# Kernel optimization log

Hardware: AMD Instinct MI355X
Metric: run time of the kernel (lower is better)

## Reference

```python
import jax, jax.numpy as jnp
import numpy as np

W = 256  # sliding_window_size


def setup_inputs() -> dict:
    key = jax.random.key(0)
    x = jax.random.normal(key, (2, 16, 4096, 64), dtype=jnp.float32)
    return {"x": x}


def _sliding_qk(q, k, w):
    """Banded QK^T, faithful to Longformer sliding_chunks_matmul_qk.
    q, k: [P, S, D]. Returns [P, S, 2w+1] with -inf at out-of-range band positions.
    """
    P, S, D = q.shape
    n = S // w  # number of w-sized chunks
    qc = q.reshape(P, n, w, D)
    # each query chunk i attends to keys in [(i-1)*w, (i+2)*w): a 3w halo window
    kp = jnp.pad(k, ((0, 0), (w, w), (0, 0)))  # pad value irrelevant, masked below
    idx = jnp.arange(n)[:, None] * w + jnp.arange(3 * w)[None, :]  # [n, 3w]
    kc = kp[:, idx, :]  # [P, n, 3w, D]
    scores = jnp.einsum('pnxd,pnyd->pnxy', qc, kc)  # [P, n, w, 3w]
    # band extraction: for row x in a chunk, offset c in [0, 2w] sits at column x + c
    gidx = jnp.arange(w)[:, None] + jnp.arange(2 * w + 1)[None, :]  # [w, 2w+1]
    band = jnp.take_along_axis(scores, gidx[None, None], axis=-1)  # [P, n, w, 2w+1]
    band = band.reshape(P, S, 2 * w + 1)
    # mask positions where key index j = i + c - w falls outside [0, S)
    i = jnp.arange(S)[:, None]
    c = jnp.arange(2 * w + 1)[None, :]
    j = i + c - w
    valid = (j >= 0) & (j < S)  # [S, 2w+1]
    return jnp.where(valid[None], band, -jnp.inf)


def reference(x):
    B, H, S, D = x.shape
    w = W
    # faithful to the torch code: transpose(1,2) then flat reshape to (B*H, S, D)
    qr = jnp.transpose(x, (0, 2, 1, 3)).reshape(B * H, S, D)
    scores = _sliding_qk(qr, qr, w)  # [B*H, S, 2w+1]
    scores = scores.reshape(B, H, S, 2 * w + 1).transpose(0, 2, 1, 3)  # [B, S, H, 2w+1]
    probs = jax.nn.softmax(scores.astype(jnp.float32), axis=-1)
    return probs.astype(x.dtype)  # dropout p=0.0 -> identity
```

## Files before the change

kernel.cpp:

```cpp
#include <hip/hip_runtime.h>
#include <math.h>

#define S_LEN 4096
#define NHEAD 16
#define WI    256
#define NC    513
#define TI    64
#define CK    96
#define NCH   6
#define NT    36
#define KSTR  72
#define PV    (S_LEN * 64)

typedef __attribute__((ext_vector_type(8))) short short8;
typedef __attribute__((ext_vector_type(4))) float floatx4;

static __device__ __forceinline__ unsigned short f2bf_rn(float f) {
  unsigned int u = __float_as_uint(f);
  u += 0x7FFFu + ((u >> 16) & 1u);
  return (unsigned short)(u >> 16);
}

__global__ __launch_bounds__(256)
void split_kernel(const float* __restrict__ x,
                  unsigned short* __restrict__ xh,
                  unsigned short* __restrict__ xl) {
  const int idx = blockIdx.x * 256 + threadIdx.x;
  const float4 val = ((const float4*)x)[idx];
  const int d4  = idx & 15;
  const int row = idx >> 4;
  const int s = row & 4095;
  const int h = (row >> 12) & 15;
  const int b = row >> 16;
  const int p = (b << 4) + (s >> 8);
  const int v = ((s & 255) << 4) + h;
  const size_t off = (size_t)p * PV + v * 64 + d4 * 4;
  const unsigned int ux = __float_as_uint(val.x), uy = __float_as_uint(val.y);
  const unsigned int uz = __float_as_uint(val.z), uw = __float_as_uint(val.w);
  ushort4 hi, lo;
  hi.x = ux >> 16; hi.y = uy >> 16; hi.z = uz >> 16; hi.w = uw >> 16;
  lo.x = f2bf_rn(val.x - __uint_as_float(ux & 0xFFFF0000u));
  lo.y = f2bf_rn(val.y - __uint_as_float(uy & 0xFFFF0000u));
  lo.z = f2bf_rn(val.z - __uint_as_float(uz & 0xFFFF0000u));
  lo.w = f2bf_rn(val.w - __uint_as_float(uw & 0xFFFF0000u));
  *(ushort4*)(xh + off) = hi;
  *(ushort4*)(xl + off) = lo;
}

__global__ __launch_bounds__(256, 2)
void attn_kernel(const unsigned short* __restrict__ xh,
                 const unsigned short* __restrict__ xl,
                 float* __restrict__ out) {
  const int t  = threadIdx.x;
  const int id = blockIdx.x;
  const int p    = id >> 6;
  const int r6   = id & 63;
  const int tile = ((r6 & 7) << 3) | (r6 >> 3);
  const int i0   = tile * TI;
  const int b    = p >> 4;
  const int hh   = p & 15;
  const int jb   = i0 - WI;
  const int w    = t >> 6;
  const int quad = (t >> 4) & 3;
  const int n    = t & 15;

  __shared__ unsigned short Qh[TI * KSTR], Ql[TI * KSTR];
  __shared__ unsigned short Kh[CK * KSTR], Kl[CK * KSTR];

  const unsigned short* ph = xh + (size_t)p * PV;
  const unsigned short* pl = xl + (size_t)p * PV;

#define LOAD_CHUNK(mm, dsth, dstl)                                      \
  { _Pragma("unroll")                                                   \
    for (int k = 0; k < 3; ++k) {                                       \
      const int u = t + (k << 8);                                       \
      const int row = u >> 3, col = (u & 7) << 3;                       \
      const int v = jb + (mm) * CK + row;                               \
      short8 zh = {0,0,0,0,0,0,0,0}, zl = {0,0,0,0,0,0,0,0};            \
      if (v >= 0 && v < S_LEN) {                                        \
        zh = *(const short8*)(ph + (size_t)v * 64 + col);               \
        zl = *(const short8*)(pl + (size_t)v * 64 + col);               \
      }                                                                 \
      (dsth)[k] = zh; (dstl)[k] = zl;                                   \
    } }

#define WRITE_CHUNK(srch, srcl)                                         \
  { _Pragma("unroll")                                                   \
    for (int k = 0; k < 3; ++k) {                                       \
      const int u = t + (k << 8);                                       \
      const int row = u >> 3, col = (u & 7) << 3;                       \
      *(short8*)(Kh + row * KSTR + col) = (srch)[k];                    \
      *(short8*)(Kl + row * KSTR + col) = (srcl)[k];                    \
    } }

  short8 qbh[2], qbl[2];
#pragma unroll
  for (int k = 0; k < 2; ++k) {
    const int u = t + (k << 8);
    const int row = u >> 3, col = (u & 7) << 3;
    qbh[k] = *(const short8*)(ph + (size_t)(i0 + row) * 64 + col);
    qbl[k] = *(const short8*)(pl + (size_t)(i0 + row) * 64 + col);
  }
  short8 pfh[2][3], pfl[2][3];
  LOAD_CHUNK(0, pfh[0], pfl[0]);
#pragma unroll
  for (int k = 0; k < 2; ++k) {
    const int u = t + (k << 8);
    const int row = u >> 3, col = (u & 7) << 3;
    *(short8*)(Qh + row * KSTR + col) = qbh[k];
    *(short8*)(Ql + row * KSTR + col) = qbl[k];
  }
  __syncthreads();

  const int arow = (w * 16 + n) * KSTR + quad * 8;
  const short8 qh0 = *(const short8*)(Qh + arow);
  const short8 qh1 = *(const short8*)(Qh + arow + 32);
  const short8 ql0 = *(const short8*)(Ql + arow);
  const short8 ql1 = *(const short8*)(Ql + arow + 32);

  floatx4 acc[NT];
#pragma unroll
  for (int jt = 0; jt < NT; ++jt) acc[jt] = (floatx4){0.f, 0.f, 0.f, 0.f};

#pragma unroll
  for (int m = 0; m < NCH; ++m) {
    WRITE_CHUNK(pfh[m & 1], pfl[m & 1]);
    __syncthreads();
    if (m < NCH - 1) LOAD_CHUNK(m + 1, pfh[(m + 1) & 1], pfl[(m + 1) & 1]);
#pragma unroll
    for (int u = 0; u < 6; ++u) {
      const int jt = m * 6 + u;
      const int kbase = (u * 16 + n) * KSTR + quad * 8;
      const short8 bh0 = *(const short8*)(Kh + kbase);
      const short8 bh1 = *(const short8*)(Kh + kbase + 32);
      const short8 bl0 = *(const short8*)(Kl + kbase);
      const short8 bl1 = *(const short8*)(Kl + kbase + 32);
      floatx4 c = acc[jt];
      c = __builtin_amdgcn_mfma_f32_16x16x32_bf16(ql0, bh0, c, 0, 0, 0);
      c = __builtin_amdgcn_mfma_f32_16x16x32_bf16(qh0, bl0, c, 0, 0, 0);
      c = __builtin_amdgcn_mfma_f32_16x16x32_bf16(qh0, bh0, c, 0, 0, 0);
      c = __builtin_amdgcn_mfma_f32_16x16x32_bf16(ql1, bh1, c, 0, 0, 0);
      c = __builtin_amdgcn_mfma_f32_16x16x32_bf16(qh1, bl1, c, 0, 0, 0);
      c = __builtin_amdgcn_mfma_f32_16x16x32_bf16(qh1, bh1, c, 0, 0, 0);
      acc[jt] = c;
    }
    if (m < NCH - 1) __syncthreads();
  }

#pragma unroll
  for (int reg = 0; reg < 4; ++reg) {
    const int o = w * 16 + quad * 4 + reg;
    const int i = i0 + o;

    float mx = acc[0][reg];
#pragma unroll
    for (int jt = 1; jt < NT; ++jt) mx = fmaxf(mx, acc[jt][reg]);
#pragma unroll
    for (int off = 1; off < 16; off <<= 1)
      mx = fmaxf(mx, __shfl_xor(mx, off, 64));

    const int A    = o - n;
    const int lo_c = (A + 15) >> 4;
    const int hi_c = (A + 512) >> 4;
    const int lo_j = (15 - jb - n) >> 4;
    const int hi_j = (4095 - jb - n) >> 4;
    const int lo   = max(lo_c, lo_j);
    const unsigned rng = (unsigned)(min(hi_c, hi_j) - lo);

    float sm = 0.f;
#pragma unroll
    for (int jt = 0; jt < NT; ++jt) {
      const bool ok = (unsigned)(jt - lo) <= rng;
      float e = __expf(acc[jt][reg] - mx);
      e = ok ? e : 0.f;
      acc[jt][reg] = e;
      sm += e;
    }
#pragma unroll
    for (int off = 1; off < 16; off <<= 1)
      sm += __shfl_xor(sm, off, 64);
    const float inv = 1.0f / sm;

    float* pb = out + (((size_t)(b * S_LEN + i) * NHEAD) + hh) * NC + (n - o);
#pragma unroll
    for (int jt = 0; jt < NT; ++jt) {
      if ((unsigned)(jt - lo) <= rng) pb[jt << 4] = acc[jt][reg] * inv;
    }
  }
#undef LOAD_CHUNK
#undef WRITE_CHUNK
}

extern "C" void kernel_launch(void* const* d_in, const int* in_sizes, int n_in,
                              void* d_out, int out_size, void* d_ws, size_t ws_size,
                              hipStream_t stream) {
  const float* x = (const float*)d_in[0];
  float* out = (float*)d_out;
  unsigned short* xh = (unsigned short*)d_ws;
  unsigned short* xl = xh + (size_t)32 * PV;

  split_kernel<<<(32 * PV / 4) / 256, 256, 0, stream>>>(x, xh, xl);
  attn_kernel<<<2048, 256, 0, stream>>>(xh, xl, out);
}
```

Measured before the change: 333.7 us.

## Halve query tile, split key tiles across warps, transpose MFMA for vector stores

The query tile per block drops from 64 to 32 rows, which doubles the grid. The four waves are now arranged 2x2, so each wave owns 16 queries and alternating key tiles, with 18 accumulators instead of 36. Occupancy rises to 3 blocks per SU and K-chunk prefetch is single-buffered. The MFMA operands are swapped so each lane holds 4 consecutive key columns, which allows float4 stores along the output row instead of strided scalar stores. The cost is extra cross-wave reductions through shared memory with syncthreads, more redundant K loading per query, and fully unaligned float4 stores because of the 513 stride.

```diff
diff --git a/kernel.cpp b/kernel.cpp
--- a/kernel.cpp
+++ b/kernel.cpp
@@ -5,15 +5,16 @@
 #define NHEAD 16
 #define WI    256
 #define NC    513
-#define TI    64
+#define TI    32
 #define CK    96
 #define NCH   6
-#define NT    36
+#define NTW   18
 #define KSTR  72
 #define PV    (S_LEN * 64)
 
 typedef __attribute__((ext_vector_type(8))) short short8;
 typedef __attribute__((ext_vector_type(4))) float floatx4;
+typedef float float4u __attribute__((ext_vector_type(4), aligned(4)));
 
 static __device__ __forceinline__ unsigned short f2bf_rn(float f) {
   unsigned int u = __float_as_uint(f);
@@ -47,25 +48,28 @@
   *(ushort4*)(xl + off) = lo;
 }
 
-__global__ __launch_bounds__(256, 2)
+__global__ __launch_bounds__(256, 3)
 void attn_kernel(const unsigned short* __restrict__ xh,
                  const unsigned short* __restrict__ xl,
                  float* __restrict__ out) {
   const int t  = threadIdx.x;
   const int id = blockIdx.x;
-  const int p    = id >> 6;
-  const int r6   = id & 63;
-  const int tile = ((r6 & 7) << 3) | (r6 >> 3);
+  const int p    = id >> 7;
+  const int r7   = id & 127;
+  const int tile = ((r7 & 7) << 4) | (r7 >> 3);
   const int i0   = tile * TI;
   const int b    = p >> 4;
   const int hh   = p & 15;
-  const int jb   = i0 - WI;
+  const int jb   = i0 - 272;
   const int w    = t >> 6;
+  const int wr   = w >> 1;
+  const int wc   = w & 1;
   const int quad = (t >> 4) & 3;
   const int n    = t & 15;
 
   __shared__ unsigned short Qh[TI * KSTR], Ql[TI * KSTR];
   __shared__ unsigned short Kh[CK * KSTR], Kl[CK * KSTR];
+  __shared__ float red[2][2][TI];
 
   const unsigned short* ph = xh + (size_t)p * PV;
   const unsigned short* pl = xl + (size_t)p * PV;
@@ -93,98 +97,106 @@
       *(short8*)(Kl + row * KSTR + col) = (srcl)[k];                    \
     } }
 
-  short8 qbh[2], qbl[2];
-#pragma unroll
-  for (int k = 0; k < 2; ++k) {
-    const int u = t + (k << 8);
-    const int row = u >> 3, col = (u & 7) << 3;
-    qbh[k] = *(const short8*)(ph + (size_t)(i0 + row) * 64 + col);
-    qbl[k] = *(const short8*)(pl + (size_t)(i0 + row) * 64 + col);
-  }
-  short8 pfh[2][3], pfl[2][3];
-  LOAD_CHUNK(0, pfh[0], pfl[0]);
-#pragma unroll
-  for (int k = 0; k < 2; ++k) {
-    const int u = t + (k << 8);
-    const int row = u >> 3, col = (u & 7) << 3;
-    *(short8*)(Qh + row * KSTR + col) = qbh[k];
-    *(short8*)(Ql + row * KSTR + col) = qbl[k];
+  short8 pfh[3], pfl[3];
+  {
+    const int row = t >> 3, col = (t & 7) << 3;
+    const short8 qbh = *(const short8*)(ph + (size_t)(i0 + row) * 64 + col);
+    const short8 qbl = *(const short8*)(pl + (size_t)(i0 + row) * 64 + col);
+    LOAD_CHUNK(0, pfh, pfl);
+    *(short8*)(Qh + row * KSTR + col) = qbh;
+    *(short8*)(Ql + row * KSTR + col) = qbl;
   }
   __syncthreads();
 
-  const int arow = (w * 16 + n) * KSTR + quad * 8;
+  const int arow = (wr * 16 + n) * KSTR + quad * 8;
   const short8 qh0 = *(const short8*)(Qh + arow);
   const short8 qh1 = *(const short8*)(Qh + arow + 32);
   const short8 ql0 = *(const short8*)(Ql + arow);
   const short8 ql1 = *(const short8*)(Ql + arow + 32);
 
-  floatx4 acc[NT];
-#pragma unroll
-  for (int jt = 0; jt < NT; ++jt) acc[jt] = (floatx4){0.f, 0.f, 0.f, 0.f};
+  floatx4 acc[NTW];
+#pragma unroll
+  for (int jt = 0; jt < NTW; ++jt) acc[jt] = (floatx4){0.f, 0.f, 0.f, 0.f};
 
 #pragma unroll
   for (int m = 0; m < NCH; ++m) {
-    WRITE_CHUNK(pfh[m & 1], pfl[m & 1]);
+    WRITE_CHUNK(pfh, pfl);
     __syncthreads();
-    if (m < NCH - 1) LOAD_CHUNK(m + 1, pfh[(m + 1) & 1], pfl[(m + 1) & 1]);
+    if (m < NCH - 1) LOAD_CHUNK(m + 1, pfh, pfl);
 #pragma unroll
     for (int u = 0; u < 6; ++u) {
-      const int jt = m * 6 + u;
+      const int g = m * 6 + u;
+      if (g == 0 || g == 35) continue;
+      if ((g & 1) != wc) continue;
+      const int jt = g >> 1;
       const int kbase = (u * 16 + n) * KSTR + quad * 8;
       const short8 bh0 = *(const short8*)(Kh + kbase);
       const short8 bh1 = *(const short8*)(Kh + kbase + 32);
       const short8 bl0 = *(const short8*)(Kl + kbase);
       const short8 bl1 = *(const short8*)(Kl + kbase + 32);
       floatx4 c = acc[jt];
-      c = __builtin_amdgcn_mfma_f32_16x16x32_bf16(ql0, bh0, c, 0, 0, 0);
-      c = __builtin_amdgcn_mfma_f32_16x16x32_bf16(qh0, bl0, c, 0, 0, 0);
-      c = __builtin_amdgcn_mfma_f32_16x16x32_bf16(qh0, bh0, c, 0, 0, 0);
-      c = __builtin_amdgcn_mfma_f32_16x16x32_bf16(ql1, bh1, c, 0, 0, 0);
-      c = __builtin_amdgcn_mfma_f32_16x16x32_bf16(qh1, bl1, c, 0, 0, 0);
-      c = __builtin_amdgcn_mfma_f32_16x16x32_bf16(qh1, bh1, c, 0, 0, 0);
+      c = __builtin_amdgcn_mfma_f32_16x16x32_bf16(bh0, ql0, c, 0, 0, 0);
+      c = __builtin_amdgcn_mfma_f32_16x16x32_bf16(bl0, qh0, c, 0, 0, 0);
+      c = __builtin_amdgcn_mfma_f32_16x16x32_bf16(bh0, qh0, c, 0, 0, 0);
+      c = __builtin_amdgcn_mfma_f32_16x16x32_bf16(bh1, ql1, c, 0, 0, 0);
+      c = __builtin_amdgcn_mfma_f32_16x16x32_bf16(bl1, qh1, c, 0, 0, 0);
+      c = __builtin_amdgcn_mfma_f32_16x16x32_bf16(bh1, qh1, c, 0, 0, 0);
       acc[jt] = c;
     }
     if (m < NCH - 1) __syncthreads();
   }
 
-#pragma unroll
-  for (int reg = 0; reg < 4; ++reg) {
-    const int o = w * 16 + quad * 4 + reg;
-    const int i = i0 + o;
-
-    float mx = acc[0][reg];
-#pragma unroll
-    for (int jt = 1; jt < NT; ++jt) mx = fmaxf(mx, acc[jt][reg]);
-#pragma unroll
-    for (int off = 1; off < 16; off <<= 1)
-      mx = fmaxf(mx, __shfl_xor(mx, off, 64));
-
-    const int A    = o - n;
-    const int lo_c = (A + 15) >> 4;
-    const int hi_c = (A + 512) >> 4;
-    const int lo_j = (15 - jb - n) >> 4;
-    const int hi_j = (4095 - jb - n) >> 4;
-    const int lo   = max(lo_c, lo_j);
-    const unsigned rng = (unsigned)(min(hi_c, hi_j) - lo);
-
-    float sm = 0.f;
-#pragma unroll
-    for (int jt = 0; jt < NT; ++jt) {
-      const bool ok = (unsigned)(jt - lo) <= rng;
+  const int i     = i0 + wr * 16 + n;
+  const int jbase = jb + 16 * wc + 4 * quad;
+  const int cbase = 16 * wc + 4 * quad - 16 * wr - n - 16;
+
+  float mx = acc[0][0];
+#pragma unroll
+  for (int jt = 0; jt < NTW; ++jt)
+#pragma unroll
+    for (int reg = 0; reg < 4; ++reg) mx = fmaxf(mx, acc[jt][reg]);
+  mx = fmaxf(mx, __shfl_xor(mx, 16, 64));
+  mx = fmaxf(mx, __shfl_xor(mx, 32, 64));
+  if (quad == 0) red[0][wc][wr * 16 + n] = mx;
+  __syncthreads();
+  mx = fmaxf(red[0][0][wr * 16 + n], red[0][1][wr * 16 + n]);
+
+  float sm = 0.f;
+#pragma unroll
+  for (int jt = 0; jt < NTW; ++jt) {
+#pragma unroll
+    for (int reg = 0; reg < 4; ++reg) {
+      const int jj = 32 * jt + jbase + reg;
+      const int cc = 32 * jt + cbase + reg;
       float e = __expf(acc[jt][reg] - mx);
+      const bool ok = ((unsigned)jj < (unsigned)S_LEN) & ((unsigned)cc <= 512u);
       e = ok ? e : 0.f;
       acc[jt][reg] = e;
       sm += e;
     }
-#pragma unroll
-    for (int off = 1; off < 16; off <<= 1)
-      sm += __shfl_xor(sm, off, 64);
-    const float inv = 1.0f / sm;
-
-    float* pb = out + (((size_t)(b * S_LEN + i) * NHEAD) + hh) * NC + (n - o);
-#pragma unroll
-    for (int jt = 0; jt < NT; ++jt) {
-      if ((unsigned)(jt - lo) <= rng) pb[jt << 4] = acc[jt][reg] * inv;
+  }
+  sm += __shfl_xor(sm, 16, 64);
+  sm += __shfl_xor(sm, 32, 64);
+  if (quad == 0) red[1][wc][wr * 16 + n] = sm;
+  __syncthreads();
+  const float inv = 1.0f / (red[1][0][wr * 16 + n] + red[1][1][wr * 16 + n]);
+
+  float* prow = out + (((size_t)(b * S_LEN + i) * NHEAD) + hh) * NC;
+#pragma unroll
+  for (int jt = 0; jt < NTW; ++jt) {
+    const int j0 = 32 * jt + jbase;
+    if ((unsigned)j0 > 4092u) continue;
+    const int c0 = 32 * jt + cbase;
+    if (c0 >= 0 && c0 <= 509) {
+      float4u v = {acc[jt][0] * inv, acc[jt][1] * inv,
+                   acc[jt][2] * inv, acc[jt][3] * inv};
+      *(float4u*)(prow + c0) = v;
+    } else if (c0 > -4 && c0 < 513) {
+#pragma unroll
+      for (int reg = 0; reg < 4; ++reg) {
+        const int cc = c0 + reg;
+        if ((unsigned)cc <= 512u) prow[cc] = acc[jt][reg] * inv;
+      }
     }
   }
 #undef LOAD_CHUNK
@@ -200,5 +212,5 @@
   unsigned short* xl = xh + (size_t)32 * PV;
 
   split_kernel<<<(32 * PV / 4) / 256, 256, 0, stream>>>(x, xh, xl);
-  attn_kernel<<<2048, 256, 0, stream>>>(xh, xl, out);
-}
+  attn_kernel<<<32 * 128, 256, 0, stream>>>(xh, xl, out);
+}
```

New measurement: 343.6 us. 1.03x slower.

## Swap MFMA operands, split key tiles across waves, skip out-of-band tiles, vectorize stores

Applied to the files above, without the earlier changes.

Reorganizes the attention kernel so each wave handles two 16-row query groups and half of the key tiles, alternating even and odd tiles. MFMA operands are swapped so every lane holds four consecutive key columns, which allows float4 output stores instead of strided scalar writes. Tiles that lie wholly outside each query group's band are skipped, and K chunks are double-buffered in LDS with a single barrier per chunk and raised wave priority during MFMA. The row max and row sum now need a cross-wave reduction through shared memory with extra barriers. The max starts from 0 rather than the true row max, which stays correct for softmax but adds some risk of precision loss.

```diff
diff --git a/kernel.cpp b/kernel.cpp
--- a/kernel.cpp
+++ b/kernel.cpp
@@ -3,17 +3,16 @@
 
 #define S_LEN 4096
 #define NHEAD 16
-#define WI    256
 #define NC    513
 #define TI    64
 #define CK    96
 #define NCH   6
-#define NT    36
 #define KSTR  72
 #define PV    (S_LEN * 64)
 
 typedef __attribute__((ext_vector_type(8))) short short8;
 typedef __attribute__((ext_vector_type(4))) float floatx4;
+typedef float float4u __attribute__((ext_vector_type(4), aligned(4)));
 
 static __device__ __forceinline__ unsigned short f2bf_rn(float f) {
   unsigned int u = __float_as_uint(f);
@@ -59,18 +58,20 @@
   const int i0   = tile * TI;
   const int b    = p >> 4;
   const int hh   = p & 15;
-  const int jb   = i0 - WI;
+  const int jb   = i0 - 256;
   const int w    = t >> 6;
+  const int wh   = w >> 1;
+  const int wc   = w & 1;
   const int quad = (t >> 4) & 3;
   const int n    = t & 15;
 
-  __shared__ unsigned short Qh[TI * KSTR], Ql[TI * KSTR];
-  __shared__ unsigned short Kh[CK * KSTR], Kl[CK * KSTR];
+  __shared__ unsigned short Kh[2][CK * KSTR], Kl[2][CK * KSTR];
+  __shared__ float red[2][2][TI];
 
   const unsigned short* ph = xh + (size_t)p * PV;
   const unsigned short* pl = xl + (size_t)p * PV;
 
-#define LOAD_CHUNK(mm, dsth, dstl)                                      \
+#define LOAD_CHUNK(mm)                                                  \
   { _Pragma("unroll")                                                   \
     for (int k = 0; k < 3; ++k) {                                       \
       const int u = t + (k << 8);                                       \
@@ -81,110 +82,150 @@
         zh = *(const short8*)(ph + (size_t)v * 64 + col);               \
         zl = *(const short8*)(pl + (size_t)v * 64 + col);               \
       }                                                                 \
-      (dsth)[k] = zh; (dstl)[k] = zl;                                   \
+      pfh[k] = zh; pfl[k] = zl;                                         \
     } }
 
-#define WRITE_CHUNK(srch, srcl)                                         \
+#define WRITE_CHUNK(buf)                                                \
   { _Pragma("unroll")                                                   \
     for (int k = 0; k < 3; ++k) {                                       \
       const int u = t + (k << 8);                                       \
       const int row = u >> 3, col = (u & 7) << 3;                       \
-      *(short8*)(Kh + row * KSTR + col) = (srch)[k];                    \
-      *(short8*)(Kl + row * KSTR + col) = (srcl)[k];                    \
+      *(short8*)(Kh[buf] + row * KSTR + col) = pfh[k];                  \
+      *(short8*)(Kl[buf] + row * KSTR + col) = pfl[k];                  \
     } }
 
-  short8 qbh[2], qbl[2];
-#pragma unroll
-  for (int k = 0; k < 2; ++k) {
-    const int u = t + (k << 8);
-    const int row = u >> 3, col = (u & 7) << 3;
-    qbh[k] = *(const short8*)(ph + (size_t)(i0 + row) * 64 + col);
-    qbl[k] = *(const short8*)(pl + (size_t)(i0 + row) * 64 + col);
-  }
-  short8 pfh[2][3], pfl[2][3];
-  LOAD_CHUNK(0, pfh[0], pfl[0]);
-#pragma unroll
-  for (int k = 0; k < 2; ++k) {
-    const int u = t + (k << 8);
-    const int row = u >> 3, col = (u & 7) << 3;
-    *(short8*)(Qh + row * KSTR + col) = qbh[k];
-    *(short8*)(Ql + row * KSTR + col) = qbl[k];
+  short8 pfh[3], pfl[3];
+
+  short8 qh[2][2], ql[2][2];
+#pragma unroll
+  for (int e = 0; e < 2; ++e) {
+    const size_t qrow = (size_t)(i0 + 16 * (2 * wh + e) + n) * 64 + quad * 8;
+    qh[e][0] = *(const short8*)(ph + qrow);
+    qh[e][1] = *(const short8*)(ph + qrow + 32);
+    ql[e][0] = *(const short8*)(pl + qrow);
+    ql[e][1] = *(const short8*)(pl + qrow + 32);
+  }
+
+  LOAD_CHUNK(0)
+  WRITE_CHUNK(0)
+  LOAD_CHUNK(1)
+  asm volatile("s_waitcnt lgkmcnt(0)" ::: "memory");
+  __builtin_amdgcn_s_barrier();
+  __builtin_amdgcn_sched_barrier(0);
+
+  floatx4 acc[2][18];
+#pragma unroll
+  for (int e = 0; e < 2; ++e)
+#pragma unroll
+    for (int jt = 0; jt < 18; ++jt) acc[e][jt] = (floatx4){0.f, 0.f, 0.f, 0.f};
+
+#pragma unroll
+  for (int m = 0; m < NCH; ++m) {
+    if (m < NCH - 1) WRITE_CHUNK((m + 1) & 1)
+    if (m < NCH - 2) LOAD_CHUNK(m + 2)
+    const unsigned short* kbh = Kh[m & 1];
+    const unsigned short* kbl = Kl[m & 1];
+    __builtin_amdgcn_s_setprio(1);
+#pragma unroll
+    for (int u6 = 0; u6 < 6; ++u6) {
+      const int g = m * 6 + u6;
+      if ((g & 1) != wc) continue;
+      const int kbase = (u6 * 16 + n) * KSTR + quad * 8;
+      const short8 bh0 = *(const short8*)(kbh + kbase);
+      const short8 bh1 = *(const short8*)(kbh + kbase + 32);
+      const short8 bl0 = *(const short8*)(kbl + kbase);
+      const short8 bl1 = *(const short8*)(kbl + kbase + 32);
+#pragma unroll
+      for (int e = 0; e < 2; ++e) {
+        const int gq = 2 * wh + e;
+        if (g < gq || g > gq + 32) continue;
+        floatx4 c = acc[e][g >> 1];
+        c = __builtin_amdgcn_mfma_f32_16x16x32_bf16(bh0, ql[e][0], c, 0, 0, 0);
+        c = __builtin_amdgcn_mfma_f32_16x16x32_bf16(bl0, qh[e][0], c, 0, 0, 0);
+        c = __builtin_amdgcn_mfma_f32_16x16x32_bf16(bh0, qh[e][0], c, 0, 0, 0);
+        c = __builtin_amdgcn_mfma_f32_16x16x32_bf16(bh1, ql[e][1], c, 0, 0, 0);
+        c = __builtin_amdgcn_mfma_f32_16x16x32_bf16(bl1, qh[e][1], c, 0, 0, 0);
+        c = __builtin_amdgcn_mfma_f32_16x16x32_bf16(bh1, qh[e][1], c, 0, 0, 0);
+        acc[e][g >> 1] = c;
+      }
+    }
+    __builtin_amdgcn_s_setprio(0);
+    asm volatile("s_waitcnt lgkmcnt(0)" ::: "memory");
+    __builtin_amdgcn_s_barrier();
+    __builtin_amdgcn_sched_barrier(0);
+  }
+
+  float mxe[2], inve[2];
+#pragma unroll
+  for (int e = 0; e < 2; ++e) {
+    float mx = 0.f;
+#pragma unroll
+    for (int jt = 0; jt < 18; ++jt)
+#pragma unroll
+      for (int rg = 0; rg < 4; ++rg) mx = fmaxf(mx, acc[e][jt][rg]);
+    mx = fmaxf(mx, __shfl_xor(mx, 16, 64));
+    mx = fmaxf(mx, __shfl_xor(mx, 32, 64));
+    if (quad == 0) red[0][wc][16 * (2 * wh + e) + n] = mx;
   }
   __syncthreads();
-
-  const int arow = (w * 16 + n) * KSTR + quad * 8;
-  const short8 qh0 = *(const short8*)(Qh + arow);
-  const short8 qh1 = *(const short8*)(Qh + arow + 32);
-  const short8 ql0 = *(const short8*)(Ql + arow);
-  const short8 ql1 = *(const short8*)(Ql + arow + 32);
-
-  floatx4 acc[NT];
-#pragma unroll
-  for (int jt = 0; jt < NT; ++jt) acc[jt] = (floatx4){0.f, 0.f, 0.f, 0.f};
-
-#pragma unroll
-  for (int m = 0; m < NCH; ++m) {
-    WRITE_CHUNK(pfh[m & 1], pfl[m & 1]);
-    __syncthreads();
-    if (m < NCH - 1) LOAD_CHUNK(m + 1, pfh[(m + 1) & 1], pfl[(m + 1) & 1]);
-#pragma unroll
-    for (int u = 0; u < 6; ++u) {
-      const int jt = m * 6 + u;
-      const int kbase = (u * 16 + n) * KSTR + quad * 8;
-      const short8 bh0 = *(const short8*)(Kh + kbase);
-      const short8 bh1 = *(const short8*)(Kh + kbase + 32);
-      const short8 bl0 = *(const short8*)(Kl + kbase);
-      const short8 bl1 = *(const short8*)(Kl + kbase + 32);
-      floatx4 c = acc[jt];
-      c = __builtin_amdgcn_mfma_f32_16x16x32_bf16(ql0, bh0, c, 0, 0, 0);
-      c = __builtin_amdgcn_mfma_f32_16x16x32_bf16(qh0, bl0, c, 0, 0, 0);
-      c = __builtin_amdgcn_mfma_f32_16x16x32_bf16(qh0, bh0, c, 0, 0, 0);
-      c = __builtin_amdgcn_mfma_f32_16x16x32_bf16(ql1, bh1, c, 0, 0, 0);
-      c = __builtin_amdgcn_mfma_f32_16x16x32_bf16(qh1, bl1, c, 0, 0, 0);
-      c = __builtin_amdgcn_mfma_f32_16x16x32_bf16(qh1, bh1, c, 0, 0, 0);
-      acc[jt] = c;
+#pragma unroll
+  for (int e = 0; e < 2; ++e) {
+    const int ridx = 16 * (2 * wh + e) + n;
+    mxe[e] = fmaxf(red[0][0][ridx], red[0][1][ridx]);
+  }
+#pragma unroll
+  for (int e = 0; e < 2; ++e) {
+    const int gq = 2 * wh + e;
+    const int cb = 16 * wc + 4 * quad - 16 * gq - n;
+    float sm = 0.f;
+#pragma unroll
+    for (int jt = 0; jt < 18; ++jt) {
+      const int j0 = jb + 32 * jt + 16 * wc + 4 * quad;
+      const int c0 = 32 * jt + cb;
+#pragma unroll
+      for (int rg = 0; rg < 4; ++rg) {
+        float ev = __expf(acc[e][jt][rg] - mxe[e]);
+        const bool ok = ((unsigned)(c0 + rg) <= 512u) &
+                        ((unsigned)(j0 + rg) < (unsigned)S_LEN);
+        ev = ok ? ev : 0.f;
+        acc[e][jt][rg] = ev;
+        sm += ev;
+      }
     }
-    if (m < NCH - 1) __syncthreads();
-  }
-
-#pragma unroll
-  for (int reg = 0; reg < 4; ++reg) {
-    const int o = w * 16 + quad * 4 + reg;
-    const int i = i0 + o;
-
-    float mx = acc[0][reg];
-#pragma unroll
-    for (int jt = 1; jt < NT; ++jt) mx = fmaxf(mx, acc[jt][reg]);
-#pragma unroll
-    for (int off = 1; off < 16; off <<= 1)
-      mx = fmaxf(mx, __shfl_xor(mx, off, 64));
-
-    const int A    = o - n;
-    const int lo_c = (A + 15) >> 4;
-    const int hi_c = (A + 512) >> 4;
-    const int lo_j = (15 - jb - n) >> 4;
-    const int hi_j = (4095 - jb - n) >> 4;
-    const int lo   = max(lo_c, lo_j);
-    const unsigned rng = (unsigned)(min(hi_c, hi_j) - lo);
-
-    float sm = 0.f;
-#pragma unroll
-    for (int jt = 0; jt < NT; ++jt) {
-      const bool ok = (unsigned)(jt - lo) <= rng;
-      float e = __expf(acc[jt][reg] - mx);
-      e = ok ? e : 0.f;
-      acc[jt][reg] = e;
-      sm += e;
-    }
-#pragma unroll
-    for (int off = 1; off < 16; off <<= 1)
-      sm += __shfl_xor(sm, off, 64);
-    const float inv = 1.0f / sm;
-
-    float* pb = out + (((size_t)(b * S_LEN + i) * NHEAD) + hh) * NC + (n - o);
-#pragma unroll
-    for (int jt = 0; jt < NT; ++jt) {
-      if ((unsigned)(jt - lo) <= rng) pb[jt << 4] = acc[jt][reg] * inv;
+    sm += __shfl_xor(sm, 16, 64);
+    sm += __shfl_xor(sm, 32, 64);
+    if (quad == 0) red[1][wc][16 * gq + n] = sm;
+  }
+  __syncthreads();
+#pragma unroll
+  for (int e = 0; e < 2; ++e) {
+    const int ridx = 16 * (2 * wh + e) + n;
+    inve[e] = 1.0f / (red[1][0][ridx] + red[1][1][ridx]);
+  }
+
+#pragma unroll
+  for (int e = 0; e < 2; ++e) {
+    const int gq  = 2 * wh + e;
+    const int i   = i0 + 16 * gq + n;
+    const int cb  = 16 * wc + 4 * quad - 16 * gq - n;
+    const float inv = inve[e];
+    float* pr = out + (((size_t)(b * S_LEN + i) * NHEAD) + hh) * NC;
+#pragma unroll
+    for (int jt = 0; jt < 18; ++jt) {
+      const int j0 = jb + 32 * jt + 16 * wc + 4 * quad;
+      if ((unsigned)j0 > 4092u) continue;
+      const int c0 = 32 * jt + cb;
+      if (c0 >= 0 && c0 <= 509) {
+        float4u v = {acc[e][jt][0] * inv, acc[e][jt][1] * inv,
+                     acc[e][jt][2] * inv, acc[e][jt][3] * inv};
+        *(float4u*)(pr + c0) = v;
+      } else if (c0 > -4 && c0 < 513) {
+#pragma unroll
+        for (int rg = 0; rg < 4; ++rg) {
+          const int cc = c0 + rg;
+          if ((unsigned)cc <= 512u) pr[cc] = acc[e][jt][rg] * inv;
+        }
+      }
     }
   }
 #undef LOAD_CHUNK
@@ -200,5 +241,5 @@
   unsigned short* xl = xh + (size_t)32 * PV;
 
   split_kernel<<<(32 * PV / 4) / 256, 256, 0, stream>>>(x, xh, xl);
-  attn_kernel<<<2048, 256, 0, stream>>>(xh, xl, out);
-}
+  attn_kernel<<<32 * 64, 256, 0, stream>>>(xh, xl, out);
+}
```

After: 354.5 us. 6.2% more time.
